# Performance work log

Hardware: AMD Instinct MI355X
Metric: run time of the kernel (lower is better)

The kernel has to match this reference:

```python
import jax, jax.numpy as jnp
import numpy as np

B, N, FA, FP, C = 64, 64, 75, 14, 128


def _mlp2(x, W0, b0, W1, b1):
    # two lazy-Linear + ReLU sub-layers (n_sub_layer=2)
    h = jax.nn.relu(x @ W0 + b0)
    return jax.nn.relu(h @ W1 + b1)


def setup_inputs() -> dict:
    key = jax.random.key(0)
    ks = jax.random.split(key, 32)
    w = lambda k, s: jax.random.normal(k, s, jnp.float32) * 0.05
    inp = {
        "atom_x": jax.random.normal(ks[0], (B, N, FA), jnp.float32),
        "pair_x": jax.random.normal(ks[1], (B, N * N, FP), jnp.float32),
        # atom_to_atom: FA -> C -> C
        "a2a_W0": w(ks[2], (FA, C)), "a2a_b0": w(ks[3], (C,)),
        "a2a_W1": w(ks[4], (C, C)), "a2a_b1": w(ks[5], (C,)),
        # pair_to_atom: FP -> C -> C
        "p2a_W0": w(ks[6], (FP, C)), "p2a_b0": w(ks[7], (C,)),
        "p2a_W1": w(ks[8], (C, C)), "p2a_b1": w(ks[9], (C,)),
        # atom_layer: 2C -> C -> C
        "al_W0": w(ks[10], (2 * C, C)), "al_b0": w(ks[11], (C,)),
        "al_W1": w(ks[12], (C, C)), "al_b1": w(ks[13], (C,)),
        # atom_to_pair (weights shared across both orderings): 2FA -> C -> C
        "a2p_W0": w(ks[14], (2 * FA, C)), "a2p_b0": w(ks[15], (C,)),
        "a2p_W1": w(ks[16], (C, C)), "a2p_b1": w(ks[17], (C,)),
        # pair_to_pair: FP -> C -> C
        "p2p_W0": w(ks[18], (FP, C)), "p2p_b0": w(ks[19], (C,)),
        "p2p_W1": w(ks[20], (C, C)), "p2p_b1": w(ks[21], (C,)),
        # pair_layer: 2C -> C -> C
        "pl_W0": w(ks[22], (2 * C, C)), "pl_b0": w(ks[23], (C,)),
        "pl_W1": w(ks[24], (C, C)), "pl_b1": w(ks[25], (C,)),
    }
    return inp


def reference(atom_x, pair_x,
              a2a_W0, a2a_b0, a2a_W1, a2a_b1,
              p2a_W0, p2a_b0, p2a_W1, p2a_b1,
              al_W0, al_b0, al_W1, al_b1,
              a2p_W0, a2p_b0, a2p_W1, a2p_b1,
              p2p_W0, p2p_b0, p2p_W1, p2p_b1,
              pl_W0, pl_b0, pl_W1, pl_b1):
    b, n, fa = atom_x.shape
    # --- atom branch ---
    a0 = _mlp2(atom_x, a2a_W0, a2a_b0, a2a_W1, a2a_b1)            # [B,N,C]
    a1 = _mlp2(pair_x, p2a_W0, p2a_b0, p2a_W1, p2a_b1)            # [B,N*N,C]
    a1 = a1.reshape(b, n, n, -1).sum(axis=2)                      # PairToAtom sum
    a = jnp.concatenate([a0, a1], axis=-1)                        # [B,N,2C]
    next_atom = jax.nn.relu(_mlp2(a, al_W0, al_b0, al_W1, al_b1))  # extra relu per forward
    # --- pair branch ---
    rep = jnp.broadcast_to(atom_x[:, None, :, :], (b, n, n, fa))  # atom_repeat
    til = jnp.broadcast_to(atom_x[:, :, None, :], (b, n, n, fa))  # atom_tile
    pr0 = jnp.concatenate([til, rep], axis=-1).reshape(b, n * n, 2 * fa)
    pr1 = jnp.concatenate([rep, til], axis=-1).reshape(b, n * n, 2 * fa)
    p0 = (_mlp2(pr0, a2p_W0, a2p_b0, a2p_W1, a2p_b1)
          + _mlp2(pr1, a2p_W0, a2p_b0, a2p_W1, a2p_b1))            # [B,N*N,C]
    p1 = _mlp2(pair_x, p2p_W0, p2p_b0, p2p_W1, p2p_b1)            # [B,N*N,C]
    p = jnp.concatenate([p0, p1], axis=-1)                        # [B,N*N,2C]
    next_pair = jax.nn.relu(_mlp2(p, pl_W0, pl_b0, pl_W1, pl_b1))
    return (next_atom, next_pair)
```

## Files before the change

### kernel.cpp

```cpp
#include <hip/hip_runtime.h>
#include <hip/hip_bf16.h>

typedef unsigned short u16;
typedef unsigned int u32;
typedef __attribute__((ext_vector_type(8))) __bf16 bf16x8;
typedef __attribute__((ext_vector_type(4))) float f32x4;

#define B_ 64
#define N_ 64
#define FA_ 75
#define FP_ 14
#define C_ 128

__device__ float g_A0[4096 * 128];
__device__ float g_A1[4096 * 128];
__device__ float g_TB[4096 * 256];
__device__ u16   g_Wf[208896];

#define OFF_PA0   53248
#define OFF_PA1   57344
#define OFF_AL0   73728
#define OFF_AL1   106496
#define OFF_AP1   122880
#define OFF_PP0   139264
#define OFF_PP1   143360
#define OFF_PL0T  159744
#define OFF_PL0B  176128
#define OFF_PL1   192512

__device__ __forceinline__ float bf2f(u16 a) {
    union { u32 u; float f; } v; v.u = ((u32)a) << 16; return v.f;
}
__device__ __forceinline__ u16 f2bf(float f) {
    union { float f; u32 u; } v; v.f = f;
    u32 r = v.u + 0x7fffu + ((v.u >> 16) & 1u);
    return (u16)(r >> 16);
}
#if __has_builtin(__builtin_amdgcn_cvt_pk_bf16_f32)
__device__ __forceinline__ u32 f2bf_pk(float a, float b) {
    auto r = __builtin_amdgcn_cvt_pk_bf16_f32(a, b);
    if constexpr (sizeof(r) == 4) {
        union { decltype(r) v; u32 u; } c; c.v = r; return c.u;
    } else {
        return (u32)f2bf(a) | ((u32)f2bf(b) << 16);
    }
}
#else
__device__ __forceinline__ u32 f2bf_pk(float a, float b) {
    return (u32)f2bf(a) | ((u32)f2bf(b) << 16);
}
#endif

__device__ __forceinline__ bool detect_isbf(const void* __restrict__ atom) {
    u32 wrd = ((const u32*)atom)[threadIdx.x & 63];
    u32 ex = (wrd >> 7) & 0xffu;
    unsigned long long m = __ballot(ex >= 113u && ex <= 133u);
    return __popcll(m) >= 32;
}

__device__ __forceinline__ float ldf(const void* p, size_t i, bool isbf) {
    if (isbf) return bf2f(((const u16*)p)[i]);
    return ((const float*)p)[i];
}
__device__ __forceinline__ f32x4 ldf4(const void* p, int i, bool isbf) {
    f32x4 r;
    if (isbf) {
        const u16* q = (const u16*)p + i;
        r[0] = bf2f(q[0]); r[1] = bf2f(q[1]); r[2] = bf2f(q[2]); r[3] = bf2f(q[3]);
    } else {
        r = *(const f32x4*)((const float*)p + i);
    }
    return r;
}
__device__ __forceinline__ uint4 pack8(const void* p, size_t base, int kmax, int k0, bool isbf) {
    uint4 u;
    if (isbf) {
        const u16* q = (const u16*)p + base;
        u16 h[8];
#pragma unroll
        for (int j = 0; j < 8; ++j) h[j] = (k0 + j < kmax) ? q[k0 + j] : (u16)0;
        u.x = (u32)h[0] | ((u32)h[1] << 16); u.y = (u32)h[2] | ((u32)h[3] << 16);
        u.z = (u32)h[4] | ((u32)h[5] << 16); u.w = (u32)h[6] | ((u32)h[7] << 16);
    } else {
        const float* q = (const float*)p + base;
        float f[8];
#pragma unroll
        for (int j = 0; j < 8; ++j) f[j] = (k0 + j < kmax) ? q[k0 + j] : 0.f;
        u.x = f2bf_pk(f[0], f[1]); u.y = f2bf_pk(f[2], f[3]);
        u.z = f2bf_pk(f[4], f[5]); u.w = f2bf_pk(f[6], f[7]);
    }
    return u;
}
__device__ __forceinline__ uint4 packW8(const void* W, int kmax, int rofft,
                                        int k0, int m, bool isbf) {
    float f[8];
#pragma unroll
    for (int j = 0; j < 8; ++j) {
        int k = k0 + j;
        f[j] = (k < kmax) ? ldf(W, (size_t)(rofft + k) * 128 + m, isbf) : 0.f;
    }
    uint4 u;
    u.x = f2bf_pk(f[0], f[1]); u.y = f2bf_pk(f[2], f[3]);
    u.z = f2bf_pk(f[4], f[5]); u.w = f2bf_pk(f[6], f[7]);
    return u;
}

__device__ __forceinline__ bf16x8 as_bf(uint4 u) {
    union { uint4 u; bf16x8 b; } cv; cv.u = u; return cv.b;
}
template<int KS, int NT>
__device__ __forceinline__ void gemm2(const u16* __restrict__ wf,
                                      const u16* __restrict__ bF,
                                      int mt0, int lane, f32x4 (&acc)[2][NT]) {
#pragma unroll
    for (int ks = 0; ks < KS; ++ks) {
        bf16x8 a0 = *(const bf16x8*)(wf + (((mt0    ) * KS + ks) * 64 + lane) * 8);
        bf16x8 a1 = *(const bf16x8*)(wf + (((mt0 + 1) * KS + ks) * 64 + lane) * 8);
#pragma unroll
        for (int nt = 0; nt < NT; ++nt) {
            bf16x8 b = *(const bf16x8*)(bF + ((nt * KS + ks) * 64 + lane) * 8);
            acc[0][nt] = __builtin_amdgcn_mfma_f32_16x16x32_bf16(a0, b, acc[0][nt], 0, 0, 0);
            acc[1][nt] = __builtin_amdgcn_mfma_f32_16x16x32_bf16(a1, b, acc[1][nt], 0, 0, 0);
        }
    }
}
template<int KS, int NT>
__device__ __forceinline__ void gemm2w(const void* W, int kmax, int rofft, bool isbf,
                                       const u16* __restrict__ bF,
                                       int mt0, int lane, f32x4 (&acc)[2][NT]) {
    const int c = lane & 15, q = lane >> 4;
#pragma unroll
    for (int ks = 0; ks < KS; ++ks) {
        int k0 = ks * 32 + q * 8;
        bf16x8 a0 = as_bf(packW8(W, kmax, rofft, k0, mt0 * 16 + c, isbf));
        bf16x8 a1 = as_bf(packW8(W, kmax, rofft, k0, (mt0 + 1) * 16 + c, isbf));
#pragma unroll
        for (int nt = 0; nt < NT; ++nt) {
            bf16x8 b = *(const bf16x8*)(bF + ((nt * KS + ks) * 64 + lane) * 8);
            acc[0][nt] = __builtin_amdgcn_mfma_f32_16x16x32_bf16(a0, b, acc[0][nt], 0, 0, 0);
            acc[1][nt] = __builtin_amdgcn_mfma_f32_16x16x32_bf16(a1, b, acc[1][nt], 0, 0, 0);
        }
    }
}
template<int KS>
__device__ __forceinline__ void loadA2(const u16* __restrict__ wf, int mt0, int lane,
                                       uint4 (&aw)[2][KS]) {
#pragma unroll
    for (int ks = 0; ks < KS; ++ks) {
        aw[0][ks] = *(const uint4*)(wf + (((mt0    ) * KS + ks) * 64 + lane) * 8);
        aw[1][ks] = *(const uint4*)(wf + (((mt0 + 1) * KS + ks) * 64 + lane) * 8);
    }
}
template<int KS, int NT>
__device__ __forceinline__ void gemm2r(const uint4 (&aw)[2][KS],
                                       const u16* __restrict__ bF,
                                       int lane, f32x4 (&acc)[2][NT]) {
#pragma unroll
    for (int ks = 0; ks < KS; ++ks) {
        bf16x8 a0 = as_bf(aw[0][ks]);
        bf16x8 a1 = as_bf(aw[1][ks]);
#pragma unroll
        for (int nt = 0; nt < NT; ++nt) {
            bf16x8 b = *(const bf16x8*)(bF + ((nt * KS + ks) * 64 + lane) * 8);
            acc[0][nt] = __builtin_amdgcn_mfma_f32_16x16x32_bf16(a0, b, acc[0][nt], 0, 0, 0);
            acc[1][nt] = __builtin_amdgcn_mfma_f32_16x16x32_bf16(a1, b, acc[1][nt], 0, 0, 0);
        }
    }
}

__device__ __forceinline__ void barrier_lgkm() {
    asm volatile("s_waitcnt lgkmcnt(0)" ::: "memory");
    __builtin_amdgcn_s_barrier();
    asm volatile("" ::: "memory");
}

__device__ __forceinline__ void frag_store(u16* dstF, int KSd, int nt, int mt, int lane, f32x4 v) {
    int c = lane & 15, quad = lane >> 4;
    int lp = c + 16 * ((2 * mt + (quad >> 1)) & 3);
    int ks = mt >> 1;
    uint2 u; u.x = f2bf_pk(v[0], v[1]); u.y = f2bf_pk(v[2], v[3]);
    *(uint2*)(dstF + (((nt * KSd + ks) * 64 + lp) * 8 + (quad & 1) * 4)) = u;
}

__device__ __forceinline__ void store_out4(void* outp, size_t elem, f32x4 v, bool isbf) {
    if (isbf) {
        uint2 u; u.x = f2bf_pk(v[0], v[1]); u.y = f2bf_pk(v[2], v[3]);
        *(uint2*)((u16*)outp + elem) = u;
    } else {
        *(f32x4*)((float*)outp + elem) = v;
    }
}

#define EPI_RELU_STORE(ACC, BB0, BB1, DST, NTN) do {                             \
    _Pragma("unroll") for (int ii = 0; ii < 2; ++ii) {                           \
        f32x4 bb_ = ii ? (BB1) : (BB0);                                          \
        _Pragma("unroll") for (int nt_ = 0; nt_ < NTN; ++nt_) {                  \
            f32x4 v_;                                                            \
            _Pragma("unroll") for (int r_ = 0; r_ < 4; ++r_) {                   \
                float x_ = ACC[ii][nt_][r_] + bb_[r_];                           \
                v_[r_] = x_ > 0.f ? x_ : 0.f;                                    \
            }                                                                    \
            frag_store(DST, 4, nt_, mt0 + ii, lane, v_);                         \
        }                                                                        \
    }                                                                            \
} while (0)

__global__ __launch_bounds__(256) void pre_fused(
    const void* atom,
    const void* aaW0, const void* aaW1, const void* apW0,
    const void* paW0, const void* paW1, const void* alW0, const void* alW1,
    const void* apW1, const void* ppW0, const void* ppW1,
    const void* plW0, const void* plW1,
    const void* aaB0, const void* aaB1) {
    __shared__ __align__(16) u16 sXF[2 * 3 * 64 * 8];
    __shared__ __align__(16) u16 sHF[2 * 4 * 64 * 8];
    const bool isbf = detect_isbf(atom);
    const int t = threadIdx.x, lane = t & 63, w = t >> 6;
    const int quad = lane >> 4;
    if (blockIdx.x < 76) {
        const void* srcs[10] = {paW0, paW1, alW0, alW1, apW1, ppW0, ppW1,
                                plW0, plW0, plW1};
        const int Ktab[10]  = {14, 128, 256, 128, 128, 14, 128, 128, 128, 128};
        const int KStab[10] = {1, 4, 8, 4, 4, 1, 4, 4, 4, 4};
        const int rofft[10] = {0, 0, 0, 0, 0, 0, 0, 0, 128, 0};
        const int baset[10] = {OFF_PA0, OFF_PA1, OFF_AL0, OFF_AL1, OFF_AP1,
                               OFF_PP0, OFF_PP1, OFF_PL0T, OFF_PL0B, OFF_PL1};
        int gid = blockIdx.x * 256 + t;
        int j = 0, s = gid;
        while (j < 10 && s >= KStab[j] * 512) { s -= KStab[j] * 512; ++j; }
        if (j >= 10) return;
        int ln = s & 63, rest = s >> 6;
        int ks = rest % KStab[j], mt = rest / KStab[j];
        int m = mt * 16 + (ln & 15), q = ln >> 4;
        float f[8];
#pragma unroll
        for (int jj = 0; jj < 8; ++jj) {
            int k = ks * 32 + q * 8 + jj;
            f[jj] = (k < Ktab[j]) ? ldf(srcs[j], (size_t)(rofft[j] + k) * 128 + m, isbf) : 0.f;
        }
        uint4 u;
        u.x = f2bf_pk(f[0], f[1]); u.y = f2bf_pk(f[2], f[3]);
        u.z = f2bf_pk(f[4], f[5]); u.w = f2bf_pk(f[6], f[7]);
        *(uint4*)&g_Wf[(size_t)baset[j] + (size_t)s * 8] = u;
        return;
    }
    const int r0g = (blockIdx.x - 76) * 32;
    for (int s = t; s < 2 * 3 * 64; s += 256) {
        int lane_s = s & 63, rest = s >> 6;
        int ks = rest % 3, nt = rest / 3;
        int n = nt * 16 + (lane_s & 15), q = lane_s >> 4;
        *(uint4*)&sXF[s * 8] = pack8(atom, (size_t)(r0g + n) * FA_, FA_, ks * 32 + q * 8, isbf);
    }
    __syncthreads();
    const int mt0 = 2 * w;
    {
        f32x4 bb0 = ldf4(aaB0, mt0 * 16 + quad * 4, isbf);
        f32x4 bb1 = ldf4(aaB0, (mt0 + 1) * 16 + quad * 4, isbf);
        f32x4 acc[2][2];
#pragma unroll
        for (int ii = 0; ii < 2; ++ii)
#pragma unroll
            for (int nt = 0; nt < 2; ++nt) acc[ii][nt] = (f32x4){0.f, 0.f, 0.f, 0.f};
        gemm2w<3, 2>(aaW0, 75, 0, isbf, sXF, mt0, lane, acc);
        EPI_RELU_STORE(acc, bb0, bb1, sHF, 2);
    }
    __syncthreads();
    {
        f32x4 bb0 = ldf4(aaB1, mt0 * 16 + quad * 4, isbf);
        f32x4 bb1 = ldf4(aaB1, (mt0 + 1) * 16 + quad * 4, isbf);
        f32x4 acc[2][2];
#pragma unroll
        for (int ii = 0; ii < 2; ++ii)
#pragma unroll
            for (int nt = 0; nt < 2; ++nt) acc[ii][nt] = (f32x4){0.f, 0.f, 0.f, 0.f};
        gemm2w<4, 2>(aaW1, 128, 0, isbf, sHF, mt0, lane, acc);
        int c = lane & 15;
#pragma unroll
        for (int ii = 0; ii < 2; ++ii) {
            int mt = mt0 + ii;
            f32x4 bb = ii ? bb1 : bb0;
#pragma unroll
            for (int nt = 0; nt < 2; ++nt) {
                f32x4 v;
#pragma unroll
                for (int r = 0; r < 4; ++r) { float x = acc[ii][nt][r] + bb[r]; v[r] = x > 0.f ? x : 0.f; }
                *(f32x4*)&g_A0[(size_t)(r0g + nt * 16 + c) * 128 + mt * 16 + quad * 4] = v;
            }
        }
    }
    {
        f32x4 accT[2][2], accB[2][2];
#pragma unroll
        for (int ii = 0; ii < 2; ++ii)
#pragma unroll
            for (int nt = 0; nt < 2; ++nt) { accT[ii][nt] = (f32x4){0.f,0.f,0.f,0.f}; accB[ii][nt] = (f32x4){0.f,0.f,0.f,0.f}; }
        gemm2w<3, 2>(apW0, 75, 0, isbf, sXF, mt0, lane, accT);
        gemm2w<3, 2>(apW0, 75, 75, isbf, sXF, mt0, lane, accB);
        int c = lane & 15;
#pragma unroll
        for (int ii = 0; ii < 2; ++ii) {
            int mt = mt0 + ii;
#pragma unroll
            for (int nt = 0; nt < 2; ++nt) {
                size_t row = (size_t)(r0g + nt * 16 + c);
                *(f32x4*)&g_TB[row * 256 + mt * 16 + quad * 4] = accT[ii][nt];
                *(f32x4*)&g_TB[row * 256 + 128 + mt * 16 + quad * 4] = accB[ii][nt];
            }
        }
    }
}

__global__ __launch_bounds__(256) void atom_layer(
    const void* __restrict__ atom,
    const void* __restrict__ alB0, const void* __restrict__ alB1,
    void* __restrict__ out) {
    __shared__ __align__(16) u16 sXF[1 * 8 * 64 * 8];
    __shared__ __align__(16) u16 sHF[1 * 4 * 64 * 8];
    const bool isbf = detect_isbf(atom);
    const int t = threadIdx.x, lane = t & 63, w = t >> 6;
    const int quad = lane >> 4;
    const int r0g = blockIdx.x * 16;
    for (int s = t; s < 8 * 64; s += 256) {
        int lane_s = s & 63, ks = s >> 6;
        int n = lane_s & 15, q = lane_s >> 4;
        int k0 = ks * 32 + q * 8;
        const float* src = (k0 < 128) ? &g_A0[(size_t)(r0g + n) * 128 + k0]
                                      : &g_A1[(size_t)(r0g + n) * 128 + (k0 - 128)];
        f32x4 f0 = *(const f32x4*)src, f1 = *(const f32x4*)(src + 4);
        uint4 u;
        u.x = f2bf_pk(f0[0], f0[1]); u.y = f2bf_pk(f0[2], f0[3]);
        u.z = f2bf_pk(f1[0], f1[1]); u.w = f2bf_pk(f1[2], f1[3]);
        *(uint4*)&sXF[s * 8] = u;
    }
    __syncthreads();
    const int mt0 = 2 * w;
    {
        f32x4 bb0 = ldf4(alB0, mt0 * 16 + quad * 4, isbf);
        f32x4 bb1 = ldf4(alB0, (mt0 + 1) * 16 + quad * 4, isbf);
        f32x4 acc[2][1];
#pragma unroll
        for (int ii = 0; ii < 2; ++ii) acc[ii][0] = (f32x4){0.f, 0.f, 0.f, 0.f};
        gemm2<8, 1>(g_Wf + OFF_AL0, sXF, mt0, lane, acc);
        EPI_RELU_STORE(acc, bb0, bb1, sHF, 1);
    }
    __syncthreads();
    {
        f32x4 bb0 = ldf4(alB1, mt0 * 16 + quad * 4, isbf);
        f32x4 bb1 = ldf4(alB1, (mt0 + 1) * 16 + quad * 4, isbf);
        f32x4 acc[2][1];
#pragma unroll
        for (int ii = 0; ii < 2; ++ii) acc[ii][0] = (f32x4){0.f, 0.f, 0.f, 0.f};
        gemm2<4, 1>(g_Wf + OFF_AL1, sHF, mt0, lane, acc);
        int c = lane & 15;
#pragma unroll
        for (int ii = 0; ii < 2; ++ii) {
            int mt = mt0 + ii;
            f32x4 bb = ii ? bb1 : bb0;
            f32x4 v;
#pragma unroll
            for (int r = 0; r < 4; ++r) { float x = acc[ii][0][r] + bb[r]; v[r] = x > 0.f ? x : 0.f; }
            store_out4(out, (size_t)(r0g + c) * 128 + mt * 16 + quad * 4, v, isbf);
        }
    }
}

__global__ __launch_bounds__(256, 3) void pair_fused(
    const void* __restrict__ atom,
    const void* __restrict__ pairx,
    const void* __restrict__ apB0, const void* __restrict__ apB1,
    const void* __restrict__ ppB0, const void* __restrict__ ppB1,
    const void* __restrict__ plB0, const void* __restrict__ plB1,
    const void* __restrict__ paB0, const void* __restrict__ paB1,
    void* __restrict__ out) {
    __shared__ __align__(16) u16 sX1[4 * 4 * 64 * 8];
    __shared__ __align__(16) u16 sX2[4 * 4 * 64 * 8];
    __shared__ __align__(16) u16 sR [4 * 4 * 64 * 8];
    __shared__ __align__(16) u16 sPr[4 * 1 * 64 * 8];
    const bool isbf = detect_isbf(atom);
    const int t = threadIdx.x, lane = t & 63, w = t >> 6;
    const int quad = lane >> 4, c = lane & 15;
    const int bx = blockIdx.x;
    const int b = bx >> 6, i = bx & 63;
    const int trow = b * 64;
    const size_t prow0 = (size_t)b * 4096 + (size_t)i * 64;
    const int mt0 = 2 * w;

    {
        int lane_s = t & 63, nt = t >> 6;
        int n = nt * 16 + (lane_s & 15), q = lane_s >> 4;
        *(uint4*)&sPr[t * 8] = pack8(pairx, (prow0 + n) * FP_, FP_, q * 8, isbf);
    }
    {
        const int ksg = t >> 6;
        const int k0 = ksg * 32 + quad * 8;
        const int rc = c;
        const float* TBi = &g_TB[(size_t)(trow + i) * 256 + k0];
        f32x4 t0 = *(const f32x4*)TBi,        t1 = *(const f32x4*)(TBi + 4);
        f32x4 o0 = *(const f32x4*)(TBi + 128), o1 = *(const f32x4*)(TBi + 132);
        f32x4 b0a = ldf4(apB0, k0, isbf), b0b = ldf4(apB0, k0 + 4, isbf);
        float Tip[8], Bip[8];
#pragma unroll
        for (int r = 0; r < 4; ++r) {
            Tip[r] = t0[r] + b0a[r]; Tip[4 + r] = t1[r] + b0b[r];
            Bip[r] = o0[r] + b0a[r]; Bip[4 + r] = o1[r] + b0b[r];
        }
#pragma unroll
        for (int nt = 0; nt < 4; ++nt) {
            int n = nt * 16 + rc;
            const float* Bj = &g_TB[(size_t)(trow + n) * 256 + k0];
            f32x4 j0 = *(const f32x4*)Bj,        j1 = *(const f32x4*)(Bj + 4);
            f32x4 j2 = *(const f32x4*)(Bj + 128), j3 = *(const f32x4*)(Bj + 132);
            float v0[8], v1[8];
#pragma unroll
            for (int r = 0; r < 4; ++r) {
                float x0 = Tip[r] + j2[r];      v0[r]     = x0 > 0.f ? x0 : 0.f;
                float x1 = Tip[4 + r] + j3[r];  v0[4 + r] = x1 > 0.f ? x1 : 0.f;
                float y0 = j0[r] + Bip[r];      v1[r]     = y0 > 0.f ? y0 : 0.f;
                float y1 = j1[r] + Bip[4 + r];  v1[4 + r] = y1 > 0.f ? y1 : 0.f;
            }
            uint4 u0, u1;
            u0.x = f2bf_pk(v0[0], v0[1]); u0.y = f2bf_pk(v0[2], v0[3]);
            u0.z = f2bf_pk(v0[4], v0[5]); u0.w = f2bf_pk(v0[6], v0[7]);
            u1.x = f2bf_pk(v1[0], v1[1]); u1.y = f2bf_pk(v1[2], v1[3]);
            u1.z = f2bf_pk(v1[4], v1[5]); u1.w = f2bf_pk(v1[6], v1[7]);
            int slot = ((nt * 4 + ksg) * 64 + lane) * 8;
            *(uint4*)&sX1[slot] = u0;
            *(uint4*)&sX2[slot] = u1;
        }
    }
    uint4 aAP1[2][4]; loadA2<4>(g_Wf + OFF_AP1, mt0, lane, aAP1);
    barrier_lgkm();
    {
        f32x4 bb0 = ldf4(apB1, mt0 * 16 + quad * 4, isbf);
        f32x4 bb1 = ldf4(apB1, (mt0 + 1) * 16 + quad * 4, isbf);
        f32x4 aA[2][4], aB[2][4];
#pragma unroll
        for (int ii = 0; ii < 2; ++ii)
#pragma unroll
            for (int nt = 0; nt < 4; ++nt) { aA[ii][nt] = (f32x4){0.f,0.f,0.f,0.f}; aB[ii][nt] = (f32x4){0.f,0.f,0.f,0.f}; }
        __builtin_amdgcn_s_setprio(1);
        gemm2r<4, 4>(aAP1, sX1, lane, aA);
        gemm2r<4, 4>(aAP1, sX2, lane, aB);
        __builtin_amdgcn_s_setprio(0);
#pragma unroll
        for (int ii = 0; ii < 2; ++ii) {
            int mt = mt0 + ii;
            f32x4 bb = ii ? bb1 : bb0;
#pragma unroll
            for (int nt = 0; nt < 4; ++nt) {
                f32x4 v;
#pragma unroll
                for (int r = 0; r < 4; ++r) {
                    float x = aA[ii][nt][r] + bb[r];
                    float y = aB[ii][nt][r] + bb[r];
                    v[r] = (x > 0.f ? x : 0.f) + (y > 0.f ? y : 0.f);
                }
                frag_store(sR, 4, nt, mt, lane, v);
            }
        }
    }
    f32x4 aH[2][4], aPA[2][4];
    {
        uint4 aPP0[2][1]; loadA2<1>(g_Wf + OFF_PP0, mt0, lane, aPP0);
        uint4 aPA0[2][1]; loadA2<1>(g_Wf + OFF_PA0, mt0, lane, aPA0);
#pragma unroll
        for (int ii = 0; ii < 2; ++ii)
#pragma unroll
            for (int nt = 0; nt < 4; ++nt) { aH[ii][nt] = (f32x4){0.f,0.f,0.f,0.f}; aPA[ii][nt] = (f32x4){0.f,0.f,0.f,0.f}; }
        gemm2r<1, 4>(aPP0, sPr, lane, aH);
        gemm2r<1, 4>(aPA0, sPr, lane, aPA);
    }
    uint4 aPL0T[2][4]; loadA2<4>(g_Wf + OFF_PL0T, mt0, lane, aPL0T);
    barrier_lgkm();
    f32x4 C3[2][4];
#pragma unroll
    for (int ii = 0; ii < 2; ++ii)
#pragma unroll
        for (int nt = 0; nt < 4; ++nt) C3[ii][nt] = (f32x4){0.f, 0.f, 0.f, 0.f};
    __builtin_amdgcn_s_setprio(1);
    gemm2r<4, 4>(aPL0T, sR, lane, C3);
    __builtin_amdgcn_s_setprio(0);
    {
        f32x4 bb0 = ldf4(ppB0, mt0 * 16 + quad * 4, isbf);
        f32x4 bb1 = ldf4(ppB0, (mt0 + 1) * 16 + quad * 4, isbf);
        EPI_RELU_STORE(aH, bb0, bb1, sX1, 4);
    }
    {
        f32x4 bb0 = ldf4(paB0, mt0 * 16 + quad * 4, isbf);
        f32x4 bb1 = ldf4(paB0, (mt0 + 1) * 16 + quad * 4, isbf);
        EPI_RELU_STORE(aPA, bb0, bb1, sX2, 4);
    }
    uint4 aPP1[2][4]; loadA2<4>(g_Wf + OFF_PP1, mt0, lane, aPP1);
    uint4 aPA1[2][4]; loadA2<4>(g_Wf + OFF_PA1, mt0, lane, aPA1);
    barrier_lgkm();
    {
        f32x4 aP[2][4], aA1[2][4];
#pragma unroll
        for (int ii = 0; ii < 2; ++ii)
#pragma unroll
            for (int nt = 0; nt < 4; ++nt) { aP[ii][nt] = (f32x4){0.f,0.f,0.f,0.f}; aA1[ii][nt] = (f32x4){0.f,0.f,0.f,0.f}; }
        __builtin_amdgcn_s_setprio(1);
        gemm2r<4, 4>(aPP1, sX1, lane, aP);
        gemm2r<4, 4>(aPA1, sX2, lane, aA1);
        __builtin_amdgcn_s_setprio(0);
        {
            f32x4 pb0 = ldf4(paB1, mt0 * 16 + quad * 4, isbf);
            f32x4 pb1 = ldf4(paB1, (mt0 + 1) * 16 + quad * 4, isbf);
#pragma unroll
            for (int ii = 0; ii < 2; ++ii) {
                int mt = mt0 + ii;
                f32x4 bb = ii ? pb1 : pb0;
                f32x4 ssum = (f32x4){0.f, 0.f, 0.f, 0.f};
#pragma unroll
                for (int nt = 0; nt < 4; ++nt)
#pragma unroll
                    for (int r = 0; r < 4; ++r) {
                        float x = aA1[ii][nt][r] + bb[r];
                        ssum[r] += (x > 0.f ? x : 0.f);
                    }
#pragma unroll
                for (int m = 1; m < 16; m <<= 1)
#pragma unroll
                    for (int r = 0; r < 4; ++r) ssum[r] += __shfl_xor(ssum[r], m, 64);
                if ((lane & 15) == 0)
                    *(f32x4*)&g_A1[(size_t)bx * 128 + mt * 16 + quad * 4] = ssum;
            }
        }
        f32x4 bb0 = ldf4(ppB1, mt0 * 16 + quad * 4, isbf);
        f32x4 bb1 = ldf4(ppB1, (mt0 + 1) * 16 + quad * 4, isbf);
        EPI_RELU_STORE(aP, bb0, bb1, sR, 4);
    }
    uint4 aPL0B[2][4]; loadA2<4>(g_Wf + OFF_PL0B, mt0, lane, aPL0B);
    barrier_lgkm();
    __builtin_amdgcn_s_setprio(1);
    gemm2r<4, 4>(aPL0B, sR, lane, C3);
    __builtin_amdgcn_s_setprio(0);
    {
        f32x4 bb0 = ldf4(plB0, mt0 * 16 + quad * 4, isbf);
        f32x4 bb1 = ldf4(plB0, (mt0 + 1) * 16 + quad * 4, isbf);
        EPI_RELU_STORE(C3, bb0, bb1, sX1, 4);
    }
    uint4 aPL1[2][4]; loadA2<4>(g_Wf + OFF_PL1, mt0, lane, aPL1);
    barrier_lgkm();
    {
        f32x4 bb0 = ldf4(plB1, mt0 * 16 + quad * 4, isbf);
        f32x4 bb1 = ldf4(plB1, (mt0 + 1) * 16 + quad * 4, isbf);
        f32x4 aO[2][4];
#pragma unroll
        for (int ii = 0; ii < 2; ++ii)
#pragma unroll
            for (int nt = 0; nt < 4; ++nt) aO[ii][nt] = (f32x4){0.f, 0.f, 0.f, 0.f};
        __builtin_amdgcn_s_setprio(1);
        gemm2r<4, 4>(aPL1, sX1, lane, aO);
        __builtin_amdgcn_s_setprio(0);
        const size_t NA = (size_t)B_ * N_ * C_;
#pragma unroll
        for (int ii = 0; ii < 2; ++ii) {
            int mt = mt0 + ii;
            f32x4 bb = ii ? bb1 : bb0;
#pragma unroll
            for (int nt = 0; nt < 4; ++nt) {
                f32x4 v;
#pragma unroll
                for (int r = 0; r < 4; ++r) { float x = aO[ii][nt][r] + bb[r]; v[r] = x > 0.f ? x : 0.f; }
                store_out4(out, NA + (prow0 + nt * 16 + c) * 128 + mt * 16 + quad * 4, v, isbf);
            }
        }
    }
}

extern "C" void kernel_launch(void* const* d_in, const int* in_sizes, int n_in,
                              void* d_out, int out_size, void* d_ws, size_t ws_size,
                              hipStream_t stream) {
    const void* atom  = d_in[0];
    const void* pairx = d_in[1];
    const void* aaW0 = d_in[2];  const void* aaB0 = d_in[3];
    const void* aaW1 = d_in[4];  const void* aaB1 = d_in[5];
    const void* paW0 = d_in[6];  const void* paB0 = d_in[7];
    const void* paW1 = d_in[8];  const void* paB1 = d_in[9];
    const void* alW0 = d_in[10]; const void* alB0 = d_in[11];
    const void* alW1 = d_in[12]; const void* alB1 = d_in[13];
    const void* apW0 = d_in[14]; const void* apB0 = d_in[15];
    const void* apW1 = d_in[16]; const void* apB1 = d_in[17];
    const void* ppW0 = d_in[18]; const void* ppB0 = d_in[19];
    const void* ppW1 = d_in[20]; const void* ppB1 = d_in[21];
    const void* plW0 = d_in[22]; const void* plB0 = d_in[23];
    const void* plW1 = d_in[24]; const void* plB1 = d_in[25];
    (void)d_ws; (void)ws_size; (void)in_sizes; (void)n_in; (void)out_size;

    pre_fused<<<204, 256, 0, stream>>>(atom, aaW0, aaW1, apW0, paW0, paW1,
                                       alW0, alW1, apW1, ppW0, ppW1, plW0, plW1,
                                       aaB0, aaB1);
    pair_fused<<<4096, 256, 0, stream>>>(atom, pairx, apB0, apB1, ppB0, ppB1,
                                         plB0, plB1, paB0, paB1, d_out);
    atom_layer<<<256, 256, 0, stream>>>(atom, alB0, alB1, d_out);
}
```

Baseline: 294.1 us.

## Fuse atom_layer into pair_fused via last-block-done atomic counters

Removes the separate atom_layer launch. Each group of 16 pair blocks that share an atom row tile bumps an atomic counter, and the last block to finish runs the two atom-layer GEMMs for that 16-row tile. The A1 partial sums are written and read with agent-scope atomics so the last block sees them. This saves a kernel launch and its tail, but adds a counter atomic, an extra barrier and a full vmcnt wait to every pair block.

```diff
diff --git a/kernel.cpp b/kernel.cpp
--- a/kernel.cpp
+++ b/kernel.cpp
@@ -16,6 +16,7 @@
 __device__ float g_A1[4096 * 128];
 __device__ float g_TB[4096 * 256];
 __device__ u16   g_Wf[208896];
+__device__ int   g_ctr16[256];
 
 #define OFF_PA0   53248
 #define OFF_PA1   57344
@@ -217,6 +218,9 @@
     const bool isbf = detect_isbf(atom);
     const int t = threadIdx.x, lane = t & 63, w = t >> 6;
     const int quad = lane >> 4;
+    if (blockIdx.x == 0) {
+        __hip_atomic_store(&g_ctr16[t], 0, __ATOMIC_RELAXED, __HIP_MEMORY_SCOPE_AGENT);
+    }
     if (blockIdx.x < 76) {
         const void* srcs[10] = {paW0, paW1, alW0, alW1, apW1, ppW0, ppW1,
                                 plW0, plW0, plW1};
@@ -310,60 +314,6 @@
     }
 }
 
-__global__ __launch_bounds__(256) void atom_layer(
-    const void* __restrict__ atom,
-    const void* __restrict__ alB0, const void* __restrict__ alB1,
-    void* __restrict__ out) {
-    __shared__ __align__(16) u16 sXF[1 * 8 * 64 * 8];
-    __shared__ __align__(16) u16 sHF[1 * 4 * 64 * 8];
-    const bool isbf = detect_isbf(atom);
-    const int t = threadIdx.x, lane = t & 63, w = t >> 6;
-    const int quad = lane >> 4;
-    const int r0g = blockIdx.x * 16;
-    for (int s = t; s < 8 * 64; s += 256) {
-        int lane_s = s & 63, ks = s >> 6;
-        int n = lane_s & 15, q = lane_s >> 4;
-        int k0 = ks * 32 + q * 8;
-        const float* src = (k0 < 128) ? &g_A0[(size_t)(r0g + n) * 128 + k0]
-                                      : &g_A1[(size_t)(r0g + n) * 128 + (k0 - 128)];
-        f32x4 f0 = *(const f32x4*)src, f1 = *(const f32x4*)(src + 4);
-        uint4 u;
-        u.x = f2bf_pk(f0[0], f0[1]); u.y = f2bf_pk(f0[2], f0[3]);
-        u.z = f2bf_pk(f1[0], f1[1]); u.w = f2bf_pk(f1[2], f1[3]);
-        *(uint4*)&sXF[s * 8] = u;
-    }
-    __syncthreads();
-    const int mt0 = 2 * w;
-    {
-        f32x4 bb0 = ldf4(alB0, mt0 * 16 + quad * 4, isbf);
-        f32x4 bb1 = ldf4(alB0, (mt0 + 1) * 16 + quad * 4, isbf);
-        f32x4 acc[2][1];
-#pragma unroll
-        for (int ii = 0; ii < 2; ++ii) acc[ii][0] = (f32x4){0.f, 0.f, 0.f, 0.f};
-        gemm2<8, 1>(g_Wf + OFF_AL0, sXF, mt0, lane, acc);
-        EPI_RELU_STORE(acc, bb0, bb1, sHF, 1);
-    }
-    __syncthreads();
-    {
-        f32x4 bb0 = ldf4(alB1, mt0 * 16 + quad * 4, isbf);
-        f32x4 bb1 = ldf4(alB1, (mt0 + 1) * 16 + quad * 4, isbf);
-        f32x4 acc[2][1];
-#pragma unroll
-        for (int ii = 0; ii < 2; ++ii) acc[ii][0] = (f32x4){0.f, 0.f, 0.f, 0.f};
-        gemm2<4, 1>(g_Wf + OFF_AL1, sHF, mt0, lane, acc);
-        int c = lane & 15;
-#pragma unroll
-        for (int ii = 0; ii < 2; ++ii) {
-            int mt = mt0 + ii;
-            f32x4 bb = ii ? bb1 : bb0;
-            f32x4 v;
-#pragma unroll
-            for (int r = 0; r < 4; ++r) { float x = acc[ii][0][r] + bb[r]; v[r] = x > 0.f ? x : 0.f; }
-            store_out4(out, (size_t)(r0g + c) * 128 + mt * 16 + quad * 4, v, isbf);
-        }
-    }
-}
-
 __global__ __launch_bounds__(256, 3) void pair_fused(
     const void* __restrict__ atom,
     const void* __restrict__ pairx,
@@ -371,11 +321,13 @@
     const void* __restrict__ ppB0, const void* __restrict__ ppB1,
     const void* __restrict__ plB0, const void* __restrict__ plB1,
     const void* __restrict__ paB0, const void* __restrict__ paB1,
+    const void* __restrict__ alB0, const void* __restrict__ alB1,
     void* __restrict__ out) {
     __shared__ __align__(16) u16 sX1[4 * 4 * 64 * 8];
     __shared__ __align__(16) u16 sX2[4 * 4 * 64 * 8];
     __shared__ __align__(16) u16 sR [4 * 4 * 64 * 8];
     __shared__ __align__(16) u16 sPr[4 * 1 * 64 * 8];
+    __shared__ int sLast;
     const bool isbf = detect_isbf(atom);
     const int t = threadIdx.x, lane = t & 63, w = t >> 6;
     const int quad = lane >> 4, c = lane & 15;
@@ -522,8 +474,13 @@
                 for (int m = 1; m < 16; m <<= 1)
 #pragma unroll
                     for (int r = 0; r < 4; ++r) ssum[r] += __shfl_xor(ssum[r], m, 64);
-                if ((lane & 15) == 0)
-                    *(f32x4*)&g_A1[(size_t)bx * 128 + mt * 16 + quad * 4] = ssum;
+                if ((lane & 15) == 0) {
+                    float* dst = &g_A1[(size_t)bx * 128 + mt * 16 + quad * 4];
+#pragma unroll
+                    for (int r = 0; r < 4; ++r)
+                        __hip_atomic_store(dst + r, ssum[r], __ATOMIC_RELAXED,
+                                           __HIP_MEMORY_SCOPE_AGENT);
+                }
             }
         }
         f32x4 bb0 = ldf4(ppB1, mt0 * 16 + quad * 4, isbf);
@@ -564,6 +521,68 @@
 #pragma unroll
                 for (int r = 0; r < 4; ++r) { float x = aO[ii][nt][r] + bb[r]; v[r] = x > 0.f ? x : 0.f; }
                 store_out4(out, NA + (prow0 + nt * 16 + c) * 128 + mt * 16 + quad * 4, v, isbf);
+            }
+        }
+    }
+    asm volatile("s_waitcnt vmcnt(0)" ::: "memory");
+    __syncthreads();
+    if (t == 0) {
+        int done = __hip_atomic_fetch_add(&g_ctr16[(b << 2) + (i >> 4)], 1,
+                                          __ATOMIC_RELAXED, __HIP_MEMORY_SCOPE_AGENT);
+        sLast = (done == 15) ? 1 : 0;
+    }
+    __syncthreads();
+    if (sLast) {
+        const int r0g = b * 64 + (i >> 4) * 16;
+        for (int s = t; s < 8 * 64; s += 256) {
+            int lane_s = s & 63, ks = s >> 6;
+            int n = lane_s & 15, q = lane_s >> 4;
+            int k0 = ks * 32 + q * 8;
+            f32x4 f0, f1;
+            if (k0 < 128) {
+                const float* src = &g_A0[(size_t)(r0g + n) * 128 + k0];
+                f0 = *(const f32x4*)src; f1 = *(const f32x4*)(src + 4);
+            } else {
+                const float* src = &g_A1[(size_t)(r0g + n) * 128 + (k0 - 128)];
+#pragma unroll
+                for (int r = 0; r < 4; ++r) {
+                    f0[r] = __hip_atomic_load(src + r, __ATOMIC_RELAXED,
+                                              __HIP_MEMORY_SCOPE_AGENT);
+                    f1[r] = __hip_atomic_load(src + 4 + r, __ATOMIC_RELAXED,
+                                              __HIP_MEMORY_SCOPE_AGENT);
+                }
+            }
+            uint4 u;
+            u.x = f2bf_pk(f0[0], f0[1]); u.y = f2bf_pk(f0[2], f0[3]);
+            u.z = f2bf_pk(f1[0], f1[1]); u.w = f2bf_pk(f1[2], f1[3]);
+            *(uint4*)&sX1[s * 8] = u;
+        }
+        __syncthreads();
+        {
+            f32x4 bb0 = ldf4(alB0, mt0 * 16 + quad * 4, isbf);
+            f32x4 bb1 = ldf4(alB0, (mt0 + 1) * 16 + quad * 4, isbf);
+            f32x4 acc[2][1];
+#pragma unroll
+            for (int ii = 0; ii < 2; ++ii) acc[ii][0] = (f32x4){0.f, 0.f, 0.f, 0.f};
+            gemm2<8, 1>(g_Wf + OFF_AL0, sX1, mt0, lane, acc);
+            EPI_RELU_STORE(acc, bb0, bb1, sX2, 1);
+        }
+        __syncthreads();
+        {
+            f32x4 bb0 = ldf4(alB1, mt0 * 16 + quad * 4, isbf);
+            f32x4 bb1 = ldf4(alB1, (mt0 + 1) * 16 + quad * 4, isbf);
+            f32x4 acc[2][1];
+#pragma unroll
+            for (int ii = 0; ii < 2; ++ii) acc[ii][0] = (f32x4){0.f, 0.f, 0.f, 0.f};
+            gemm2<4, 1>(g_Wf + OFF_AL1, sX2, mt0, lane, acc);
+#pragma unroll
+            for (int ii = 0; ii < 2; ++ii) {
+                int mt = mt0 + ii;
+                f32x4 bb = ii ? bb1 : bb0;
+                f32x4 v;
+#pragma unroll
+                for (int r = 0; r < 4; ++r) { float x = acc[ii][0][r] + bb[r]; v[r] = x > 0.f ? x : 0.f; }
+                store_out4(out, (size_t)(r0g + c) * 128 + mt * 16 + quad * 4, v, isbf);
             }
         }
     }
@@ -592,6 +611,5 @@
                                        alW0, alW1, apW1, ppW0, ppW1, plW0, plW1,
                                        aaB0, aaB1);
     pair_fused<<<4096, 256, 0, stream>>>(atom, pairx, apB0, apB1, ppB0, ppB1,
-                                         plB0, plB1, paB0, paB1, d_out);
-    atom_layer<<<256, 256, 0, stream>>>(atom, alB0, alB1, d_out);
-}
+                                         plB0, plB1, paB0, paB1, alB0, alB1, d_out);
+}
```

New measurement: 350.4 us. +19.1%, slower.
